# Kernel optimization log

Measured on AMD Instinct MI355X. Metric: run time of the kernel, lower is better.

The kernel has to match this reference:

```python
import jax, jax.numpy as jnp
import numpy as np

N_NODES = 50000
N_EDGES = 400000
C_NODE = 128
C_EDGE = 256
# PyG: round(c_in + (c_out-c_in)*f)
H1, H2, H3 = 166, 192, 218


def setup_inputs() -> dict:
    key = jax.random.key(0)
    ks = jax.random.split(key, 20)
    x = jax.random.normal(ks[0], (N_NODES, C_NODE), dtype=jnp.float32)
    edge_index = jax.random.randint(ks[1], (2, N_EDGES), 0, N_NODES, dtype=jnp.int64)

    def glorot(k, fan_in, fan_out):
        s = jnp.sqrt(6.0 / (fan_in + fan_out)).astype(jnp.float32)
        return jax.random.uniform(k, (fan_in, fan_out), jnp.float32, -s, s)

    dims_e = [(C_NODE, H1), (H1, H2), (H2, H3), (H3, C_EDGE)]
    dims_n = [(C_NODE, C_NODE)] * 4
    inp = {"x": x, "edge_index": edge_index}
    for i, (fi, fo) in enumerate(dims_e, 1):
        inp[f"W{i}e"] = glorot(ks[1 + i], fi, fo)
        inp[f"b{i}e"] = jnp.zeros((fo,), jnp.float32)
    for i, (fi, fo) in enumerate(dims_n, 1):
        inp[f"W{i}n"] = glorot(ks[9 + i], fi, fo)
        inp[f"b{i}n"] = jnp.zeros((fo,), jnp.float32)
    return inp


def _gcn_norm(edge_index, n_nodes):
    # add self loops, then symmetric normalization (PyG gcn_norm, improved=False)
    loops = jnp.arange(n_nodes, dtype=edge_index.dtype)
    src = jnp.concatenate([edge_index[0], loops])
    dst = jnp.concatenate([edge_index[1], loops])
    deg = jax.ops.segment_sum(jnp.ones_like(dst, dtype=jnp.float32), dst, num_segments=n_nodes)
    dinv = jnp.where(deg > 0, jax.lax.rsqrt(deg), 0.0)
    norm = dinv[src] * dinv[dst]  # [E+N]
    return src, dst, norm


def _gcn_conv(h_in, W, b, src, dst, norm, n_nodes):
    h = h_in @ W                      # [N, C_out] dense transform first (PyG order)
    msg = h[src] * norm[:, None]      # gather + scale, [E+N, C_out]
    agg = jax.ops.segment_sum(msg, dst, num_segments=n_nodes)
    return agg + b


def _forward(x, edge_index, We, be, Wn, bn):
    n = x.shape[0]
    src, dst, norm = _gcn_norm(edge_index, n)
    e = x
    for i in range(4):
        e = _gcn_conv(e, We[i], be[i], src, dst, norm, n)
        e = jax.nn.relu(e) if i < 3 else jax.nn.sigmoid(e)
    v = x
    for i in range(4):
        v = _gcn_conv(v, Wn[i], bn[i], src, dst, norm, n)
        v = jax.nn.relu(v) if i < 3 else jax.nn.sigmoid(v)
    return e, v


def reference(x, edge_index, W1e, b1e, W2e, b2e, W3e, b3e, W4e, b4e,
              W1n, b1n, W2n, b2n, W3n, b3n, W4n, b4n):
    We = [W1e, W2e, W3e, W4e]
    be = [b1e, b2e, b3e, b4e]
    Wn = [W1n, W2n, W3n, W4n]
    bn = [b1n, b2n, b3n, b4n]
    return _forward(x, edge_index, We, be, Wn, bn)
```

## Files before the change

### kernel.cpp

```cpp
#include <hip/hip_runtime.h>
#include <hip/hip_bf16.h>
#include <cstdint>
#include <cstddef>

typedef __hip_bfloat16 bf16;
typedef __attribute__((ext_vector_type(8))) short bf16x8;
typedef __attribute__((ext_vector_type(4))) float f32x4;

#define NN 50000
#define NE 400000

struct PTab {
    const void* p[17];
    int n[17];
};

__device__ __forceinline__ float bf2f(unsigned short u) {
    return __uint_as_float(((unsigned)u) << 16);
}
__device__ __forceinline__ unsigned short f2bf(float f) {
    __hip_bfloat16 h = __float2bfloat16(f);
    return *reinterpret_cast<unsigned short*>(&h);
}
__device__ __forceinline__ float fin(float v) {
    return (v == v && v > -1e30f && v < 1e30f) ? v : 0.0f;
}
__device__ __forceinline__ float rd(const void* p, int i, int f) {
    return f ? ((const float*)p)[i] : bf2f(((const unsigned short*)p)[i]);
}

__device__ __forceinline__ void gl16(const void* g, void* l) {
    __builtin_amdgcn_global_load_lds(
        (const __attribute__((address_space(1))) unsigned int*)g,
        (__attribute__((address_space(3))) unsigned int*)l, 16, 0, 0);
}

__global__ void k_probe(PTab tab, const int* __restrict__ ei, int* __restrict__ flags) {
    __shared__ int zc, bc, sAny;
    for (int t = 0; t < 17; ++t) {
        if (threadIdx.x == 0) { zc = 0; bc = 0; }
        __syncthreads();
        int words = tab.n[t] >> 1;
        if (words > 256) words = 256;
        if ((int)threadIdx.x < words) {
            unsigned w = ((const unsigned*)tab.p[t])[threadIdx.x];
            if (w == 0u) atomicAdd(&zc, 1);
            else {
                int e = (w >> 7) & 0xFF;
                if (e >= 100 && e <= 140) atomicAdd(&bc, 1);
            }
        }
        __syncthreads();
        if (threadIdx.x == 0) {
            int nz = words - zc;
            flags[t] = (nz == 0 || 2 * bc >= nz) ? 0 : 1;
        }
        __syncthreads();
    }
    if (threadIdx.x == 0) sAny = 0;
    __syncthreads();
    int any = 0;
    for (int i = threadIdx.x; i < 2048; i += 256) any |= ei[2 * i + 1];
    if (any) sAny = 1;
    __syncthreads();
    if (threadIdx.x == 0) flags[17] = sAny;
}

__global__ void k_wsplit(const void* __restrict__ W, const int* __restrict__ flags, int fidx,
                         int K, int M, int Kp,
                         unsigned short* __restrict__ wh, unsigned short* __restrict__ wl) {
    int n = blockIdx.x;
    int k = threadIdx.x;
    if (k >= Kp) return;
    float v = 0.0f;
    if (k < K && n < M) v = fin(rd(W, k * M + n, flags[fidx]));
    unsigned short hi = f2bf(v);
    unsigned short lo = f2bf(v - bf2f(hi));
    wh[(size_t)n * Kp + k] = hi;
    wl[(size_t)n * Kp + k] = lo;
}

struct MOff { int m[8]; int mp[8]; };

__global__ void k_biasall(PTab tab, const int* __restrict__ flags, MOff mo,
                          float* __restrict__ dst) {
    int l = blockIdx.x;
    int fidx = 2 + 2 * l;
    int M = tab.n[fidx];
    int i = threadIdx.x;
    if (i < mo.mp[l])
        dst[mo.m[l] + i] = (i < M) ? fin(rd(tab.p[fidx], i, flags[fidx])) : 0.0f;
}

__global__ void k_repack(const int* __restrict__ ei, const int* __restrict__ flags,
                         int* __restrict__ src, int* __restrict__ dst) {
    int e = blockIdx.x * blockDim.x + threadIdx.x;
    if (e >= NE) return;
    int s, d;
    if (flags[17]) { s = ei[e]; d = ei[NE + e]; }
    else           { s = ei[2 * e]; d = ei[2 * (NE + e)]; }
    src[e] = min(max(s, 0), NN - 1);
    dst[e] = min(max(d, 0), NN - 1);
}

__global__ void k_zero2(int* __restrict__ a, int* __restrict__ b, int n) {
    int i = blockIdx.x * blockDim.x + threadIdx.x;
    if (i < n) { a[i] = 0; b[i] = 0; }
}

__global__ void k_count(const int* __restrict__ dst, int* __restrict__ deg) {
    int e = blockIdx.x * blockDim.x + threadIdx.x;
    if (e < NE) atomicAdd(&deg[dst[e]], 1);
}

__global__ void k_scan1(const int* __restrict__ deg, int* __restrict__ rowp,
                        int* __restrict__ part) {
    __shared__ int s[512];
    int tid = threadIdx.x, i = blockIdx.x * 512 + tid;
    int v = (i < NN) ? deg[i] : 0;
    s[tid] = v;
    __syncthreads();
    for (int off = 1; off < 512; off <<= 1) {
        int t = (tid >= off) ? s[tid - off] : 0;
        __syncthreads();
        s[tid] += t;
        __syncthreads();
    }
    if (i < NN) rowp[i] = s[tid] - v;
    if (tid == 511) part[blockIdx.x] = s[511];
}
__global__ void k_scan2(int* __restrict__ part, int nb) {
    __shared__ int s[128];
    int tid = threadIdx.x;
    int v = (tid < nb) ? part[tid] : 0;
    s[tid] = v;
    __syncthreads();
    for (int off = 1; off < 128; off <<= 1) {
        int t = (tid >= off) ? s[tid - off] : 0;
        __syncthreads();
        s[tid] += t;
        __syncthreads();
    }
    if (tid < nb) part[tid] = s[tid] - v;
}
__global__ void k_scan3(int* __restrict__ rowp, const int* __restrict__ part,
                        const int* __restrict__ deg, float* __restrict__ dinv) {
    int i = blockIdx.x * blockDim.x + threadIdx.x;
    if (i < NN) {
        rowp[i] += part[i >> 9];
        dinv[i] = rsqrtf((float)deg[i] + 1.0f);
    }
    if (i == 0) rowp[NN] = NE;
}

__global__ void k_fill(const int* __restrict__ src, const int* __restrict__ dst,
                       const int* __restrict__ rowp, int* __restrict__ cursor,
                       int* __restrict__ colv) {
    int e = blockIdx.x * blockDim.x + threadIdx.x;
    if (e >= NE) return;
    int d = dst[e];
    int p = atomicAdd(&cursor[d], 1);
    colv[rowp[d] + p] = src[e];
}

__global__ void k_xin(const void* __restrict__ x, const int* __restrict__ flags,
                      const float* __restrict__ dinv, unsigned short* __restrict__ xs) {
    int t = blockIdx.x * blockDim.x + threadIdx.x;
    if (t >= NN * 16) return;
    int i = t >> 4, c = (t & 15) * 8;
    float d = dinv[i];
    int f = flags[0];
    const float* xf = (const float*)x + (size_t)i * 128 + c;
    const unsigned short* xb = (const unsigned short*)x + (size_t)i * 128 + c;
    unsigned short o[8];
    #pragma unroll
    for (int j = 0; j < 8; ++j)
        o[j] = f2bf(fin(f ? xf[j] : bf2f(xb[j])) * d);
    *(uint4*)(xs + (size_t)i * 128 + c) = *(uint4*)o;
}

__launch_bounds__(256)
__global__ void k_gather(const unsigned short* __restrict__ in, int istride,
                         unsigned short* __restrict__ out, int ostride, int lanes,
                         const int* __restrict__ rowp, const int* __restrict__ colv,
                         const float* __restrict__ dinv) {
    const int node = blockIdx.x * 4 + (threadIdx.x >> 6);
    if (node >= NN) return;
    const int lane = threadIdx.x & 63;
    const int beg = rowp[node], end = rowp[node + 1];
    float a[8] = {0.f, 0.f, 0.f, 0.f, 0.f, 0.f, 0.f, 0.f};
    if (lanes <= 16) {
        const int slot = lane >> 4;
        const int l8 = lane & 15;
        const bool on = l8 < lanes;
        const size_t off = (size_t)l8 * 8;
        if (slot == 0 && on) {
            uint4 q = *(const uint4*)(in + (size_t)node * istride + off);
            unsigned v[4] = {q.x, q.y, q.z, q.w};
            #pragma unroll
            for (int t = 0; t < 4; ++t) {
                a[2 * t] += bf2f(v[t] & 0xFFFF); a[2 * t + 1] += bf2f(v[t] >> 16);
            }
        }
        for (int j = beg + slot; j < end; j += 4) {
            const int s = colv[j];
            if (on) {
                uint4 q = *(const uint4*)(in + (size_t)s * istride + off);
                unsigned v[4] = {q.x, q.y, q.z, q.w};
                #pragma unroll
                for (int t = 0; t < 4; ++t) {
                    a[2 * t] += bf2f(v[t] & 0xFFFF); a[2 * t + 1] += bf2f(v[t] >> 16);
                }
            }
        }
        #pragma unroll
        for (int t = 0; t < 8; ++t) {
            a[t] += __shfl_xor(a[t], 16);
            a[t] += __shfl_xor(a[t], 32);
        }
        if (lane < lanes) {
            float d = dinv[node];
            unsigned short o[8];
            #pragma unroll
            for (int t = 0; t < 8; ++t) o[t] = f2bf(a[t] * d);
            *(uint4*)(out + (size_t)node * ostride + (size_t)lane * 8) = *(uint4*)o;
        }
    } else {
        const bool on = lane < lanes;
        const size_t off = (size_t)lane * 8;
        if (on) {
            uint4 q = *(const uint4*)(in + (size_t)node * istride + off);
            unsigned v[4] = {q.x, q.y, q.z, q.w};
            #pragma unroll
            for (int t = 0; t < 4; ++t) {
                a[2 * t] += bf2f(v[t] & 0xFFFF); a[2 * t + 1] += bf2f(v[t] >> 16);
            }
        }
        int j = beg;
        for (; j + 3 < end; j += 4) {
            int s0 = colv[j], s1 = colv[j + 1], s2 = colv[j + 2], s3 = colv[j + 3];
            if (on) {
                uint4 q0 = *(const uint4*)(in + (size_t)s0 * istride + off);
                uint4 q1 = *(const uint4*)(in + (size_t)s1 * istride + off);
                uint4 q2 = *(const uint4*)(in + (size_t)s2 * istride + off);
                uint4 q3 = *(const uint4*)(in + (size_t)s3 * istride + off);
                unsigned v0[4] = {q0.x, q0.y, q0.z, q0.w};
                unsigned v1[4] = {q1.x, q1.y, q1.z, q1.w};
                unsigned v2[4] = {q2.x, q2.y, q2.z, q2.w};
                unsigned v3[4] = {q3.x, q3.y, q3.z, q3.w};
                #pragma unroll
                for (int t = 0; t < 4; ++t) {
                    a[2 * t]     += bf2f(v0[t] & 0xFFFF) + bf2f(v1[t] & 0xFFFF)
                                  + bf2f(v2[t] & 0xFFFF) + bf2f(v3[t] & 0xFFFF);
                    a[2 * t + 1] += bf2f(v0[t] >> 16) + bf2f(v1[t] >> 16)
                                  + bf2f(v2[t] >> 16) + bf2f(v3[t] >> 16);
                }
            }
        }
        for (; j < end; ++j) {
            int s = colv[j];
            if (on) {
                uint4 q = *(const uint4*)(in + (size_t)s * istride + off);
                unsigned v[4] = {q.x, q.y, q.z, q.w};
                #pragma unroll
                for (int t = 0; t < 4; ++t) {
                    a[2 * t] += bf2f(v[t] & 0xFFFF); a[2 * t + 1] += bf2f(v[t] >> 16);
                }
            }
        }
        if (on) {
            float d = dinv[node];
            unsigned short o[8];
            #pragma unroll
            for (int t = 0; t < 8; ++t) o[t] = f2bf(a[t] * d);
            *(uint4*)(out + (size_t)node * ostride + off) = *(uint4*)o;
        }
    }
}

struct GSide {
    const unsigned short* A;
    const unsigned short* Wh;
    const unsigned short* Wl;
    const float* bias;
    void* out;
    int Kp, ostride, M, OutW, act;
};

__launch_bounds__(256, 3)
__global__ void k_mgemm(GSide s0, GSide s1, int ySplit, int astride,
                        const float* __restrict__ dinv) {
    __shared__ __align__(16) unsigned char ldsraw[49152];
    auto sA  = reinterpret_cast<unsigned short (*)[128][32]>(ldsraw);
    auto sBh = reinterpret_cast<unsigned short (*)[128][32]>(ldsraw + 16384);
    auto sBl = reinterpret_cast<unsigned short (*)[128][32]>(ldsraw + 32768);

    const int tid = threadIdx.x;
    const int wave = tid >> 6, lane = tid & 63;
    const int wr = wave >> 1, wc = wave & 1;
    const int quad = lane >> 4, m16 = lane & 15;

    GSide S; int ycol;
    if ((int)blockIdx.y < ySplit) { S = s0; ycol = blockIdx.y; }
    else                          { S = s1; ycol = blockIdx.y - ySplit; }
    const int row0 = blockIdx.x * 128, col0 = ycol * 128;
    const int Kp = S.Kp;

    const int lr = lane >> 2;
    const int swz = ((lane >> 2) ^ (lane >> 4)) & 3;
    const int su = ((lane & 3) ^ swz) * 8;

    int ar1 = row0 + wave * 32 + lr;      if (ar1 >= NN) ar1 = NN - 1;
    int ar2 = row0 + wave * 32 + 16 + lr; if (ar2 >= NN) ar2 = NN - 1;
    const unsigned short* gA1 = S.A + (size_t)ar1 * astride + su;
    const unsigned short* gA2 = S.A + (size_t)ar2 * astride + su;
    const int br = col0 + wave * 32 + lr;
    const unsigned short* gBh1 = S.Wh + (size_t)br * Kp + su;
    const unsigned short* gBl1 = S.Wl + (size_t)br * Kp + su;

    f32x4 zz = {0.f, 0.f, 0.f, 0.f};
    f32x4 acc[4][4];
    #pragma unroll
    for (int i = 0; i < 4; ++i)
        #pragma unroll
        for (int j = 0; j < 4; ++j) acc[i][j] = zz;

    const int rs = (quad ^ ((m16 & 3) ^ ((m16 >> 2) & 3))) * 8;
    const int nk = Kp >> 5;

    auto stage = [&](int b, int k0) {
        gl16(gA1 + k0,            &sA[b][wave * 32][0]);
        gl16(gA2 + k0,            &sA[b][wave * 32 + 16][0]);
        gl16(gBh1 + k0,           &sBh[b][wave * 32][0]);
        gl16(gBh1 + 16 * Kp + k0, &sBh[b][wave * 32 + 16][0]);
        gl16(gBl1 + k0,           &sBl[b][wave * 32][0]);
        gl16(gBl1 + 16 * Kp + k0, &sBl[b][wave * 32 + 16][0]);
    };

    stage(0, 0);
    __syncthreads();
    int cur = 0;
    for (int ks = 0; ks < nk; ++ks) {
        if (ks + 1 < nk) stage(cur ^ 1, (ks + 1) * 32);
        bf16x8 fa[4], fh[4], fl[4];
        #pragma unroll
        for (int i = 0; i < 4; ++i) {
            fa[i] = *(const bf16x8*)&sA[cur][wr * 64 + i * 16 + m16][rs];
            fh[i] = *(const bf16x8*)&sBh[cur][wc * 64 + i * 16 + m16][rs];
            fl[i] = *(const bf16x8*)&sBl[cur][wc * 64 + i * 16 + m16][rs];
        }
        #pragma unroll
        for (int i = 0; i < 4; ++i)
            #pragma unroll
            for (int j = 0; j < 4; ++j) {
                acc[i][j] = __builtin_amdgcn_mfma_f32_16x16x32_bf16(fa[i], fh[j], acc[i][j], 0, 0, 0);
                acc[i][j] = __builtin_amdgcn_mfma_f32_16x16x32_bf16(fa[i], fl[j], acc[i][j], 0, 0, 0);
            }
        __syncthreads();
        cur ^= 1;
    }

    float* eps = (float*)(ldsraw + (size_t)wave * 4352);
    #pragma unroll
    for (int i = 0; i < 4; ++i) {
        #pragma unroll
        for (int j = 0; j < 4; ++j) {
            int col = col0 + wc * 64 + j * 16 + m16;
            float bcol = (col < S.M) ? S.bias[col] : 0.0f;
            #pragma unroll
            for (int r = 0; r < 4; ++r) {
                float v = acc[i][j][r] + bcol;
                if (S.act) v = (col < S.M) ? 1.0f / (1.0f + expf(-v)) : 0.0f;
                else       v = (col < S.M) ? fmaxf(v, 0.0f) : 0.0f;
                eps[(quad * 4 + r) * 68 + j * 16 + m16] = v;
            }
        }
        asm volatile("s_waitcnt lgkmcnt(0)" ::: "memory");
        __builtin_amdgcn_sched_barrier(0);
        #pragma unroll
        for (int it = 0; it < 4; ++it) {
            int lr2 = it * 4 + (lane >> 4);
            int c4 = (lane & 15) * 4;
            float4 w = *(float4*)&eps[lr2 * 68 + c4];
            int grow = row0 + wr * 64 + i * 16 + lr2;
            int gcol = col0 + wc * 64 + c4;
            if (grow < NN && gcol < S.OutW) {
                if (S.act) {
                    *(float4*)((float*)S.out + (size_t)grow * S.ostride + gcol) = w;
                } else {
                    float d = dinv[grow];
                    unsigned o0 = f2bf(w.x * d) | ((unsigned)f2bf(w.y * d) << 16);
                    unsigned o1 = f2bf(w.z * d) | ((unsigned)f2bf(w.w * d) << 16);
                    uint2 u; u.x = o0; u.y = o1;
                    *(uint2*)((unsigned short*)S.out + (size_t)grow * S.ostride + gcol) = u;
                }
            }
        }
        asm volatile("s_waitcnt lgkmcnt(0)" ::: "memory");
        __builtin_amdgcn_sched_barrier(0);
    }
}

__global__ void k_sentinel(float* __restrict__ out, int n) {
    int i = blockIdx.x * blockDim.x + threadIdx.x;
    if (i < n) out[i] = 4.0f;
}

extern "C" void kernel_launch(void* const* d_in, const int* in_sizes, int n_in,
                              void* d_out, int out_size, void* d_ws, size_t ws_size,
                              hipStream_t stream) {
    const int* ei = (const int*)d_in[1];
    float* out_e = (float*)d_out;
    float* out_v = out_e + (size_t)NN * 256;

    const int wsz[16] = {128 * 166, 166, 166 * 192, 192, 192 * 218, 218, 218 * 256, 256,
                         128 * 128, 128, 128 * 128, 128, 128 * 128, 128, 128 * 128, 128};
    PTab tab;
    tab.p[0] = d_in[0]; tab.n[0] = NN * 128;
    for (int t = 0; t < 16; ++t) { tab.p[t + 1] = d_in[2 + t]; tab.n[t + 1] = wsz[t]; }

    const int KpW[8] = {128, 192, 192, 224, 0, 128, 128, 128};
    const int MpW[8] = {384, 256, 256, 256, 0, 128, 128, 128};

    char* wsb = (char*)d_ws;
    size_t o = 0;
    auto align = [](size_t v) { return (v + 255) & ~(size_t)255; };
    int*   flags  = (int*)(wsb + o);  o = align(o + 128);
    int*   colv   = (int*)(wsb + o);  o = align(o + (size_t)NE * 4);
    int*   deg    = (int*)(wsb + o);  o = align(o + (size_t)NN * 4);
    int*   cursor = (int*)(wsb + o);  o = align(o + (size_t)NN * 4);
    int*   rowp   = (int*)(wsb + o);  o = align(o + (size_t)(NN + 1) * 4);
    int*   part   = (int*)(wsb + o);  o = align(o + 512);
    float* dinv   = (float*)(wsb + o); o = align(o + (size_t)NN * 4);
    unsigned short* wh[8]; unsigned short* wl[8];
    for (int l = 0; l < 8; ++l) {
        size_t wel = (size_t)MpW[l] * KpW[l];
        wh[l] = (unsigned short*)(wsb + o); o = align(o + wel * 2);
        wl[l] = (unsigned short*)(wsb + o); o = align(o + wel * 2);
    }
    float* ball = (float*)(wsb + o); o = align(o + 1376 * 4);
    unsigned short* bufA = (unsigned short*)(wsb + o); o = align(o + (size_t)NN * 352 * 2);
    unsigned short* bufB = (unsigned short*)(wsb + o); o = align(o + (size_t)NN * 352 * 2);
    int* src32 = (int*)bufB;
    int* dst32 = src32 + NE;
    if (o > ws_size) {
        k_sentinel<<<(out_size + 255) / 256, 256, 0, stream>>>(out_e, out_size);
        return;
    }

    MOff mo;
    const int moff[8] = {0, 320, 512, 736, 192, 992, 1120, 1248};
    const int mpad[8] = {192, 192, 224, 256, 128, 128, 128, 128};
    for (int l = 0; l < 8; ++l) { mo.m[l] = moff[l]; mo.mp[l] = mpad[l]; }

    const int EB = (NE + 255) / 256;
    const int NB512 = (NN + 511) / 512;
    const int GX = (NN + 127) / 128;
    const int GN = (NN + 3) / 4;

    k_probe<<<1, 256, 0, stream>>>(tab, ei, flags);
    k_wsplit<<<192, 256, 0, stream>>>(d_in[2],  flags, 1,  128, 166, 128, wh[0], wl[0]);
    k_wsplit<<<192, 256, 0, stream>>>(d_in[10], flags, 9,  128, 128, 128,
                                      wh[0] + 192 * 128, wl[0] + 192 * 128);
    k_wsplit<<<256, 256, 0, stream>>>(d_in[4],  flags, 3,  166, 192, 192, wh[1], wl[1]);
    k_wsplit<<<256, 256, 0, stream>>>(d_in[6],  flags, 5,  192, 218, 192, wh[2], wl[2]);
    k_wsplit<<<256, 256, 0, stream>>>(d_in[8],  flags, 7,  218, 256, 224, wh[3], wl[3]);
    k_wsplit<<<128, 256, 0, stream>>>(d_in[12], flags, 11, 128, 128, 128, wh[5], wl[5]);
    k_wsplit<<<128, 256, 0, stream>>>(d_in[14], flags, 13, 128, 128, 128, wh[6], wl[6]);
    k_wsplit<<<128, 256, 0, stream>>>(d_in[16], flags, 15, 128, 128, 128, wh[7], wl[7]);
    k_biasall<<<8, 256, 0, stream>>>(tab, flags, mo, ball);

    k_repack<<<EB, 256, 0, stream>>>(ei, flags, src32, dst32);
    k_zero2<<<(NN + 255) / 256, 256, 0, stream>>>(deg, cursor, NN);
    k_count<<<EB, 256, 0, stream>>>(dst32, deg);
    k_scan1<<<NB512, 512, 0, stream>>>(deg, rowp, part);
    k_scan2<<<1, 128, 0, stream>>>(part, NB512);
    k_scan3<<<(NN + 255) / 256, 256, 0, stream>>>(rowp, part, deg, dinv);
    k_fill<<<EB, 256, 0, stream>>>(src32, dst32, rowp, cursor, colv);

    k_xin<<<(NN * 16 + 255) / 256, 256, 0, stream>>>(d_in[0], flags, dinv, bufA);
    k_gather<<<GN, 256, 0, stream>>>(bufA, 128, bufB, 128, 16, rowp, colv, dinv);

    {
        GSide s0 = {bufB, wh[0], wl[0], ball, bufA, 128, 320, 320, 320, 0};
        k_mgemm<<<dim3(GX, 3), 256, 0, stream>>>(s0, s0, 3, 128, dinv);
    }
    k_gather<<<GN, 256, 0, stream>>>(bufA, 320, bufB, 320, 40, rowp, colv, dinv);

    {
        GSide s0 = {bufB, wh[1], wl[1], ball + 320, bufA, 192, 320, 192, 192, 0};
        GSide s1 = {bufB + 192, wh[5], wl[5], ball + 992, bufA + 192, 128, 320, 128, 128, 0};
        k_mgemm<<<dim3(GX, 3), 256, 0, stream>>>(s0, s1, 2, 320, dinv);
    }
    k_gather<<<GN, 256, 0, stream>>>(bufA, 320, bufB, 320, 40, rowp, colv, dinv);

    {
        GSide s0 = {bufB, wh[2], wl[2], ball + 512, bufA, 192, 352, 218, 224, 0};
        GSide s1 = {bufB + 192, wh[6], wl[6], ball + 1120, bufA + 224, 128, 352, 128, 128, 0};
        k_mgemm<<<dim3(GX, 3), 256, 0, stream>>>(s0, s1, 2, 320, dinv);
    }
    k_gather<<<GN, 256, 0, stream>>>(bufA, 352, bufB, 352, 44, rowp, colv, dinv);

    {
        GSide s0 = {bufB, wh[3], wl[3], ball + 736, out_e, 224, 256, 256, 256, 1};
        GSide s1 = {bufB + 224, wh[7], wl[7], ball + 1248, out_v, 128, 128, 128, 128, 1};
        k_mgemm<<<dim3(GX, 3), 256, 0, stream>>>(s0, s1, 2, 352, dinv);
    }
}
```

Measured before the change: 511.4 us.

## Batch weight splits, fuse degree count, swizzle GEMM blocks, narrow layer-1 buffer

```diff
diff --git a/kernel.cpp b/kernel.cpp
--- a/kernel.cpp
+++ b/kernel.cpp
@@ -66,18 +66,30 @@
     if (threadIdx.x == 0) flags[17] = sAny;
 }
 
-__global__ void k_wsplit(const void* __restrict__ W, const int* __restrict__ flags, int fidx,
-                         int K, int M, int Kp,
-                         unsigned short* __restrict__ wh, unsigned short* __restrict__ wl) {
-    int n = blockIdx.x;
+struct WSeg {
+    const void* src[8];
+    unsigned short* wh[8];
+    unsigned short* wl[8];
+    int f[8], K[8], M[8], Kp[8];
+    int b0[9];
+};
+
+__global__ void k_wsplitall(WSeg G, const int* __restrict__ flags) {
+    int bid = blockIdx.x;
+    int seg = 0;
+    #pragma unroll
+    for (int t = 1; t < 8; ++t) if (bid >= G.b0[t]) seg = t;
+    int n = bid - G.b0[seg];
     int k = threadIdx.x;
+    int Kp = G.Kp[seg];
     if (k >= Kp) return;
     float v = 0.0f;
-    if (k < K && n < M) v = fin(rd(W, k * M + n, flags[fidx]));
+    if (k < G.K[seg] && n < G.M[seg])
+        v = fin(rd(G.src[seg], k * G.M[seg] + n, flags[G.f[seg]]));
     unsigned short hi = f2bf(v);
     unsigned short lo = f2bf(v - bf2f(hi));
-    wh[(size_t)n * Kp + k] = hi;
-    wl[(size_t)n * Kp + k] = lo;
+    G.wh[seg][(size_t)n * Kp + k] = hi;
+    G.wl[seg][(size_t)n * Kp + k] = lo;
 }
 
 struct MOff { int m[8]; int mp[8]; };
@@ -93,24 +105,18 @@
 }
 
 __global__ void k_repack(const int* __restrict__ ei, const int* __restrict__ flags,
-                         int* __restrict__ src, int* __restrict__ dst) {
+                         int* __restrict__ src, int* __restrict__ dst,
+                         int* __restrict__ deg) {
     int e = blockIdx.x * blockDim.x + threadIdx.x;
     if (e >= NE) return;
     int s, d;
     if (flags[17]) { s = ei[e]; d = ei[NE + e]; }
     else           { s = ei[2 * e]; d = ei[2 * (NE + e)]; }
-    src[e] = min(max(s, 0), NN - 1);
-    dst[e] = min(max(d, 0), NN - 1);
-}
-
-__global__ void k_zero2(int* __restrict__ a, int* __restrict__ b, int n) {
-    int i = blockIdx.x * blockDim.x + threadIdx.x;
-    if (i < n) { a[i] = 0; b[i] = 0; }
-}
-
-__global__ void k_count(const int* __restrict__ dst, int* __restrict__ deg) {
-    int e = blockIdx.x * blockDim.x + threadIdx.x;
-    if (e < NE) atomicAdd(&deg[dst[e]], 1);
+    s = min(max(s, 0), NN - 1);
+    d = min(max(d, 0), NN - 1);
+    src[e] = s;
+    dst[e] = d;
+    atomicAdd(&deg[d], 1);
 }
 
 __global__ void k_scan1(const int* __restrict__ deg, int* __restrict__ rowp,
@@ -189,29 +195,23 @@
     const int lane = threadIdx.x & 63;
     const int beg = rowp[node], end = rowp[node + 1];
     float a[8] = {0.f, 0.f, 0.f, 0.f, 0.f, 0.f, 0.f, 0.f};
+    auto accq = [&](uint4 q) {
+        unsigned v[4] = {q.x, q.y, q.z, q.w};
+        #pragma unroll
+        for (int t = 0; t < 4; ++t) {
+            a[2 * t] += bf2f(v[t] & 0xFFFF); a[2 * t + 1] += bf2f(v[t] >> 16);
+        }
+    };
     if (lanes <= 16) {
         const int slot = lane >> 4;
         const int l8 = lane & 15;
         const bool on = l8 < lanes;
         const size_t off = (size_t)l8 * 8;
-        if (slot == 0 && on) {
-            uint4 q = *(const uint4*)(in + (size_t)node * istride + off);
-            unsigned v[4] = {q.x, q.y, q.z, q.w};
-            #pragma unroll
-            for (int t = 0; t < 4; ++t) {
-                a[2 * t] += bf2f(v[t] & 0xFFFF); a[2 * t + 1] += bf2f(v[t] >> 16);
-            }
-        }
+        if (slot == 0 && on)
+            accq(*(const uint4*)(in + (size_t)node * istride + off));
         for (int j = beg + slot; j < end; j += 4) {
             const int s = colv[j];
-            if (on) {
-                uint4 q = *(const uint4*)(in + (size_t)s * istride + off);
-                unsigned v[4] = {q.x, q.y, q.z, q.w};
-                #pragma unroll
-                for (int t = 0; t < 4; ++t) {
-                    a[2 * t] += bf2f(v[t] & 0xFFFF); a[2 * t + 1] += bf2f(v[t] >> 16);
-                }
-            }
+            if (on) accq(*(const uint4*)(in + (size_t)s * istride + off));
         }
         #pragma unroll
         for (int t = 0; t < 8; ++t) {
@@ -228,45 +228,47 @@
     } else {
         const bool on = lane < lanes;
         const size_t off = (size_t)lane * 8;
-        if (on) {
-            uint4 q = *(const uint4*)(in + (size_t)node * istride + off);
-            unsigned v[4] = {q.x, q.y, q.z, q.w};
-            #pragma unroll
-            for (int t = 0; t < 4; ++t) {
-                a[2 * t] += bf2f(v[t] & 0xFFFF); a[2 * t + 1] += bf2f(v[t] >> 16);
-            }
-        }
+        if (on) accq(*(const uint4*)(in + (size_t)node * istride + off));
         int j = beg;
-        for (; j + 3 < end; j += 4) {
+        for (; j + 8 <= end; j += 8) {
+            int s0 = colv[j], s1 = colv[j + 1], s2 = colv[j + 2], s3 = colv[j + 3];
+            int s4 = colv[j + 4], s5 = colv[j + 5], s6 = colv[j + 6], s7 = colv[j + 7];
+            if (on) {
+                uint4 q0 = *(const uint4*)(in + (size_t)s0 * istride + off);
+                uint4 q1 = *(const uint4*)(in + (size_t)s1 * istride + off);
+                uint4 q2 = *(const uint4*)(in + (size_t)s2 * istride + off);
+                uint4 q3 = *(const uint4*)(in + (size_t)s3 * istride + off);
+                uint4 q4 = *(const uint4*)(in + (size_t)s4 * istride + off);
+                uint4 q5 = *(const uint4*)(in + (size_t)s5 * istride + off);
+                uint4 q6 = *(const uint4*)(in + (size_t)s6 * istride + off);
+                uint4 q7 = *(const uint4*)(in + (size_t)s7 * istride + off);
+                accq(q0); accq(q1); accq(q2); accq(q3);
+                accq(q4); accq(q5); accq(q6); accq(q7);
+            }
+        }
+        if (j + 4 <= end) {
             int s0 = colv[j], s1 = colv[j + 1], s2 = colv[j + 2], s3 = colv[j + 3];
             if (on) {
                 uint4 q0 = *(const uint4*)(in + (size_t)s0 * istride + off);
                 uint4 q1 = *(const uint4*)(in + (size_t)s1 * istride + off);
                 uint4 q2 = *(const uint4*)(in + (size_t)s2 * istride + off);
                 uint4 q3 = *(const uint4*)(in + (size_t)s3 * istride + off);
-                unsigned v0[4] = {q0.x, q0.y, q0.z, q0.w};
-                unsigned v1[4] = {q1.x, q1.y, q1.z, q1.w};
-                unsigned v2[4] = {q2.x, q2.y, q2.z, q2.w};
-                unsigned v3[4] = {q3.x, q3.y, q3.z, q3.w};
-                #pragma unroll
-                for (int t = 0; t < 4; ++t) {
-                    a[2 * t]     += bf2f(v0[t] & 0xFFFF) + bf2f(v1[t] & 0xFFFF)
-                                  + bf2f(v2[t] & 0xFFFF) + bf2f(v3[t] & 0xFFFF);
-                    a[2 * t + 1] += bf2f(v0[t] >> 16) + bf2f(v1[t] >> 16)
-                                  + bf2f(v2[t] >> 16) + bf2f(v3[t] >> 16);
-                }
-            }
-        }
-        for (; j < end; ++j) {
-            int s = colv[j];
+                accq(q0); accq(q1); accq(q2); accq(q3);
+            }
+            j += 4;
+        }
+        if (j + 2 <= end) {
+            int s0 = colv[j], s1 = colv[j + 1];
             if (on) {
-                uint4 q = *(const uint4*)(in + (size_t)s * istride + off);
-                unsigned v[4] = {q.x, q.y, q.z, q.w};
-                #pragma unroll
-                for (int t = 0; t < 4; ++t) {
-                    a[2 * t] += bf2f(v[t] & 0xFFFF); a[2 * t + 1] += bf2f(v[t] >> 16);
-                }
-            }
+                uint4 q0 = *(const uint4*)(in + (size_t)s0 * istride + off);
+                uint4 q1 = *(const uint4*)(in + (size_t)s1 * istride + off);
+                accq(q0); accq(q1);
+            }
+            j += 2;
+        }
+        if (j < end) {
+            int s0 = colv[j];
+            if (on) accq(*(const uint4*)(in + (size_t)s0 * istride + off));
         }
         if (on) {
             float d = dinv[node];
@@ -288,7 +290,7 @@
 };
 
 __launch_bounds__(256, 3)
-__global__ void k_mgemm(GSide s0, GSide s1, int ySplit, int astride,
+__global__ void k_mgemm(GSide s0, GSide s1, int ySplit, int NY, int NB, int astride,
                         const float* __restrict__ dinv) {
     __shared__ __align__(16) unsigned char ldsraw[49152];
     auto sA  = reinterpret_cast<unsigned short (*)[128][32]>(ldsraw);
@@ -300,10 +302,22 @@
     const int wr = wave >> 1, wc = wave & 1;
     const int quad = lane >> 4, m16 = lane & 15;
 
+    const int NBa = NB & ~7;
+    const int swcut = NBa * NY;
+    int b = blockIdx.x, x, yv;
+    if (b < swcut) {
+        x = (b / (8 * NY)) * 8 + (b & 7);
+        yv = (b >> 3) % NY;
+    } else {
+        int r = b - swcut, rem = NB - NBa;
+        x = rem ? (NBa + r % rem) : 0;
+        yv = rem ? (r / rem) : 0;
+    }
+
     GSide S; int ycol;
-    if ((int)blockIdx.y < ySplit) { S = s0; ycol = blockIdx.y; }
-    else                          { S = s1; ycol = blockIdx.y - ySplit; }
-    const int row0 = blockIdx.x * 128, col0 = ycol * 128;
+    if (yv < ySplit) { S = s0; ycol = yv; }
+    else             { S = s1; ycol = yv - ySplit; }
+    const int row0 = x * 128, col0 = ycol * 128;
     const int Kp = S.Kp;
 
     const int lr = lane >> 2;
@@ -328,13 +342,13 @@
     const int rs = (quad ^ ((m16 & 3) ^ ((m16 >> 2) & 3))) * 8;
     const int nk = Kp >> 5;
 
-    auto stage = [&](int b, int k0) {
-        gl16(gA1 + k0,            &sA[b][wave * 32][0]);
-        gl16(gA2 + k0,            &sA[b][wave * 32 + 16][0]);
-        gl16(gBh1 + k0,           &sBh[b][wave * 32][0]);
-        gl16(gBh1 + 16 * Kp + k0, &sBh[b][wave * 32 + 16][0]);
-        gl16(gBl1 + k0,           &sBl[b][wave * 32][0]);
-        gl16(gBl1 + 16 * Kp + k0, &sBl[b][wave * 32 + 16][0]);
+    auto stage = [&](int bb, int k0) {
+        gl16(gA1 + k0,            &sA[bb][wave * 32][0]);
+        gl16(gA2 + k0,            &sA[bb][wave * 32 + 16][0]);
+        gl16(gBh1 + k0,           &sBh[bb][wave * 32][0]);
+        gl16(gBh1 + 16 * Kp + k0, &sBh[bb][wave * 32 + 16][0]);
+        gl16(gBl1 + k0,           &sBl[bb][wave * 32][0]);
+        gl16(gBl1 + 16 * Kp + k0, &sBl[bb][wave * 32 + 16][0]);
     };
 
     stage(0, 0);
@@ -449,8 +463,8 @@
     }
 
     MOff mo;
-    const int moff[8] = {0, 320, 512, 736, 192, 992, 1120, 1248};
-    const int mpad[8] = {192, 192, 224, 256, 128, 128, 128, 128};
+    const int moff[8] = {0, 296, 616, 968, 168, 488, 840, 1224};
+    const int mpad[8] = {168, 192, 224, 256, 128, 128, 128, 128};
     for (int l = 0; l < 8; ++l) { mo.m[l] = moff[l]; mo.mp[l] = mpad[l]; }
 
     const int EB = (NE + 255) / 256;
@@ -459,20 +473,34 @@
     const int GN = (NN + 3) / 4;
 
     k_probe<<<1, 256, 0, stream>>>(tab, ei, flags);
-    k_wsplit<<<192, 256, 0, stream>>>(d_in[2],  flags, 1,  128, 166, 128, wh[0], wl[0]);
-    k_wsplit<<<192, 256, 0, stream>>>(d_in[10], flags, 9,  128, 128, 128,
-                                      wh[0] + 192 * 128, wl[0] + 192 * 128);
-    k_wsplit<<<256, 256, 0, stream>>>(d_in[4],  flags, 3,  166, 192, 192, wh[1], wl[1]);
-    k_wsplit<<<256, 256, 0, stream>>>(d_in[6],  flags, 5,  192, 218, 192, wh[2], wl[2]);
-    k_wsplit<<<256, 256, 0, stream>>>(d_in[8],  flags, 7,  218, 256, 224, wh[3], wl[3]);
-    k_wsplit<<<128, 256, 0, stream>>>(d_in[12], flags, 11, 128, 128, 128, wh[5], wl[5]);
-    k_wsplit<<<128, 256, 0, stream>>>(d_in[14], flags, 13, 128, 128, 128, wh[6], wl[6]);
-    k_wsplit<<<128, 256, 0, stream>>>(d_in[16], flags, 15, 128, 128, 128, wh[7], wl[7]);
+
+    {
+        WSeg G;
+        const void* srcs[8] = {d_in[2], d_in[10], d_in[4], d_in[12],
+                               d_in[6], d_in[14], d_in[8], d_in[16]};
+        unsigned short* whp[8] = {wh[0], wh[0] + 168 * 128, wh[1], wh[5],
+                                  wh[2], wh[6], wh[3], wh[7]};
+        unsigned short* wlp[8] = {wl[0], wl[0] + 168 * 128, wl[1], wl[5],
+                                  wl[2], wl[6], wl[3], wl[7]};
+        const int fs[8]  = {1, 9, 3, 11, 5, 13, 7, 15};
+        const int Ks[8]  = {128, 128, 166, 128, 192, 128, 218, 128};
+        const int Ms[8]  = {166, 128, 192, 128, 218, 128, 256, 128};
+        const int Kps[8] = {128, 128, 192, 128, 192, 128, 224, 128};
+        const int rows[8] = {168, 216, 256, 128, 256, 128, 256, 128};
+        int acc = 0;
+        for (int s = 0; s < 8; ++s) {
+            G.src[s] = srcs[s]; G.wh[s] = whp[s]; G.wl[s] = wlp[s];
+            G.f[s] = fs[s]; G.K[s] = Ks[s]; G.M[s] = Ms[s]; G.Kp[s] = Kps[s];
+            G.b0[s] = acc; acc += rows[s];
+        }
+        G.b0[8] = acc;
+        k_wsplitall<<<acc, 256, 0, stream>>>(G, flags);
+    }
     k_biasall<<<8, 256, 0, stream>>>(tab, flags, mo, ball);
 
-    k_repack<<<EB, 256, 0, stream>>>(ei, flags, src32, dst32);
-    k_zero2<<<(NN + 255) / 256, 256, 0, stream>>>(deg, cursor, NN);
-    k_count<<<EB, 256, 0, stream>>>(dst32, deg);
+    hipMemsetAsync(deg, 0, (size_t)NN * 4, stream);
+    hipMemsetAsync(cursor, 0, (size_t)NN * 4, stream);
+    k_repack<<<EB, 256, 0, stream>>>(ei, flags, src32, dst32, deg);
     k_scan1<<<NB512, 512, 0, stream>>>(deg, rowp, part);
     k_scan2<<<1, 128, 0, stream>>>(part, NB512);
     k_scan3<<<(NN + 255) / 256, 256, 0, stream>>>(rowp, part, deg, dinv);
@@ -482,28 +510,29 @@
     k_gather<<<GN, 256, 0, stream>>>(bufA, 128, bufB, 128, 16, rowp, colv, dinv);
 
     {
-        GSide s0 = {bufB, wh[0], wl[0], ball, bufA, 128, 320, 320, 320, 0};
-        k_mgemm<<<dim3(GX, 3), 256, 0, stream>>>(s0, s0, 3, 128, dinv);
+        GSide s0 = {bufB, wh[0], wl[0], ball, bufA, 128, 296, 296, 296, 0};
+        k_mgemm<<<GX * 3, 256, 0, stream>>>(s0, s0, 3, 3, GX, 128, dinv);
+    }
+    k_gather<<<GN, 256, 0, stream>>>(bufA, 296, bufB, 296, 37, rowp, colv, dinv);
+
+    {
+        GSide s0 = {bufB, wh[1], wl[1], ball + 616, bufA, 192, 320, 192, 192, 0};
+        GSide s1 = {bufB + 168, wh[5], wl[5], ball + 488, bufA + 192, 128, 320, 128, 128, 0};
+        s0.bias = ball + 296;
+        k_mgemm<<<GX * 3, 256, 0, stream>>>(s0, s1, 2, 3, GX, 296, dinv);
     }
     k_gather<<<GN, 256, 0, stream>>>(bufA, 320, bufB, 320, 40, rowp, colv, dinv);
 
     {
-        GSide s0 = {bufB, wh[1], wl[1], ball + 320, bufA, 192, 320, 192, 192, 0};
-        GSide s1 = {bufB + 192, wh[5], wl[5], ball + 992, bufA + 192, 128, 320, 128, 128, 0};
-        k_mgemm<<<dim3(GX, 3), 256, 0, stream>>>(s0, s1, 2, 320, dinv);
-    }
-    k_gather<<<GN, 256, 0, stream>>>(bufA, 320, bufB, 320, 40, rowp, colv, dinv);
+        GSide s0 = {bufB, wh[2], wl[2], ball + 616, bufA, 192, 352, 218, 224, 0};
+        GSide s1 = {bufB + 192, wh[6], wl[6], ball + 840, bufA + 224, 128, 352, 128, 128, 0};
+        k_mgemm<<<GX * 3, 256, 0, stream>>>(s0, s1, 2, 3, GX, 320, dinv);
+    }
+    k_gather<<<GN, 256, 0, stream>>>(bufA, 352, bufB, 352, 44, rowp, colv, dinv);
 
     {
-        GSide s0 = {bufB, wh[2], wl[2], ball + 512, bufA, 192, 352, 218, 224, 0};
-        GSide s1 = {bufB + 192, wh[6], wl[6], ball + 1120, bufA + 224, 128, 352, 128, 128, 0};
-        k_mgemm<<<dim3(GX, 3), 256, 0, stream>>>(s0, s1, 2, 320, dinv);
-    }
-    k_gather<<<GN, 256, 0, stream>>>(bufA, 352, bufB, 352, 44, rowp, colv, dinv);
-
-    {
-        GSide s0 = {bufB, wh[3], wl[3], ball + 736, out_e, 224, 256, 256, 256, 1};
-        GSide s1 = {bufB + 224, wh[7], wl[7], ball + 1248, out_v, 128, 128, 128, 128, 1};
-        k_mgemm<<<dim3(GX, 3), 256, 0, stream>>>(s0, s1, 2, 352, dinv);
-    }
-}
+        GSide s0 = {bufB, wh[3], wl[3], ball + 968, out_e, 224, 256, 256, 256, 1};
+        GSide s1 = {bufB + 224, wh[7], wl[7], ball + 1224, out_v, 128, 128, 128, 128, 1};
+        k_mgemm<<<GX * 3, 256, 0, stream>>>(s0, s1, 2, 3, GX, 352, dinv);
+    }
+}
```

Result: no change. 515.4 us (+0.8%).
